# Kernel tuning notes

Measured on AMD Instinct MI355X. Metric: run time of the kernel, lower is better.

Reference implementation:

```python
import jax, jax.numpy as jnp
import numpy as np

N, E, G = 50000, 500000, 32
H, D = 4, 40  # heads, per-head dim; hidden = H*D = 160
HID, JK = H * D, 2 * H * D  # 160, 320


def setup_inputs() -> dict:
    key = jax.random.key(0)
    ks = jax.random.split(key, 32)
    s = 0.05
    inp = {
        'x': jax.random.normal(ks[0], (N, 5), jnp.float32),
        'edge_index': jax.random.randint(ks[1], (2, E), 0, N, jnp.int32).astype(jnp.int64),
        'edge_attr': jax.random.normal(ks[2], (E, 4), jnp.float32),
        'batch': jnp.sort(jax.random.randint(ks[3], (N,), 0, G, jnp.int32)).astype(jnp.int64),
        'W_in': jax.random.normal(ks[4], (5, HID), jnp.float32) * s,
        'b_in': jnp.zeros((HID,), jnp.float32),
        'Wq': jax.random.normal(ks[5], (2, HID, HID), jnp.float32) * s,
        'bq': jnp.zeros((2, HID), jnp.float32),
        'Wk': jax.random.normal(ks[6], (2, HID, HID), jnp.float32) * s,
        'bk': jnp.zeros((2, HID), jnp.float32),
        'Wv': jax.random.normal(ks[7], (2, HID, HID), jnp.float32) * s,
        'bv': jnp.zeros((2, HID), jnp.float32),
        'We': jax.random.normal(ks[8], (2, 4, HID), jnp.float32) * s,
        'be': jnp.zeros((2, HID), jnp.float32),
        'Wskip': jax.random.normal(ks[9], (2, HID, HID), jnp.float32) * s,
        'bskip': jnp.zeros((2, HID), jnp.float32),
        'Wbeta': jax.random.normal(ks[10], (2, 3 * HID, 1), jnp.float32) * s,
        'Wg1': jax.random.normal(ks[11], (JK, JK // 2), jnp.float32) * s,
        'bg1': jnp.zeros((JK // 2,), jnp.float32),
        'Wg2': jax.random.normal(ks[12], (JK // 2, 1), jnp.float32) * s,
        'bg2': jnp.zeros((1,), jnp.float32),
        'Wh1': jax.random.normal(ks[13], (JK, JK), jnp.float32) * s,
        'bh1': jnp.zeros((JK,), jnp.float32),
        'Wh2': jax.random.normal(ks[14], (JK, 6), jnp.float32) * s,
        'bh2': jnp.zeros((6,), jnp.float32),
    }
    return inp


def _transformer_conv(h, src, dst, edge_attr, Wq, bq, Wk, bk, Wv, bv, We, be, Wskip, bskip, Wbeta):
    n = h.shape[0]
    q = (h @ Wq + bq).reshape(n, H, D)
    k = (h @ Wk + bk).reshape(n, H, D)
    v = (h @ Wv + bv).reshape(n, H, D)
    e = (edge_attr @ We + be).reshape(-1, H, D)   # [E,H,D]
    k_e = k[src] + e                              # key with edge feature
    v_e = v[src] + e                              # value with edge feature
    alpha = jnp.einsum('ehd,ehd->eh', q[dst], k_e) / jnp.sqrt(jnp.float32(D))  # [E,H]
    # segment softmax over incoming edges of each destination node
    amax = jax.ops.segment_max(alpha, dst, num_segments=n)
    ex = jnp.exp(alpha - amax[dst])
    denom = jax.ops.segment_sum(ex, dst, num_segments=n)
    a = ex / denom[dst]                           # [E,H]
    out = jax.ops.segment_sum(v_e * a[..., None], dst, num_segments=n).reshape(n, H * D)
    # beta gate with skip connection
    r = h @ Wskip + bskip
    beta = jax.nn.sigmoid(jnp.concatenate([out, r, out - r], axis=-1) @ Wbeta)  # [n,1]
    return beta * r + (1.0 - beta) * out


def reference(x, edge_index, edge_attr, batch, W_in, b_in, Wq, bq, Wk, bk, Wv, bv,
              We, be, Wskip, bskip, Wbeta, Wg1, bg1, Wg2, bg2, Wh1, bh1, Wh2, bh2):
    src, dst = edge_index[0], edge_index[1]
    h = x @ W_in + b_in
    xs = []
    for l in range(2):
        h = _transformer_conv(h, src, dst, edge_attr, Wq[l], bq[l], Wk[l], bk[l],
                              Wv[l], bv[l], We[l], be[l], Wskip[l], bskip[l], Wbeta[l])
        xs.append(h)
    xc = jnp.concatenate(xs, axis=-1)             # JumpingKnowledge 'cat' -> [N,320]
    # AttentionalAggregation: gate MLP + segment softmax over graphs
    gate = jax.nn.relu(xc @ Wg1 + bg1) @ Wg2 + bg2  # [N,1]
    gmax = jax.ops.segment_max(gate, batch, num_segments=G)
    ge = jnp.exp(gate - gmax[batch])
    gden = jax.ops.segment_sum(ge, batch, num_segments=G)
    att = ge / gden[batch]
    pooled = jax.ops.segment_sum(att * xc, batch, num_segments=G)  # [G,320]
    out = jax.nn.relu(pooled @ Wh1 + bh1) @ Wh2 + bh2              # [G,6]
    return out.reshape(-1, 2, 3)
```

## Files before the change

### kernel.cpp

```cpp
#include <hip/hip_runtime.h>
#include <math.h>
#include <stddef.h>

#define NHEAD 4
#define DHEAD 40
#define HIDW 160
#define JKW 320
#define NGRAPH 32
#define BCAP 64

typedef __attribute__((ext_vector_type(8))) short short8;
typedef __attribute__((ext_vector_type(4))) float f32x4;
typedef __attribute__((ext_vector_type(2))) float f32x2;
typedef __fp16 h2 __attribute__((ext_vector_type(2)));
typedef int i32x4 __attribute__((ext_vector_type(4)));
typedef i32x4 i32x4_a4 __attribute__((aligned(4)));

__device__ inline unsigned short f2bf(float x){
  unsigned u = __float_as_uint(x);
  u += 0x7fff + ((u >> 16) & 1);
  return (unsigned short)(u >> 16);
}
__device__ inline float bf2f(unsigned short h){
  return __uint_as_float(((unsigned)h) << 16);
}
__device__ inline float fdot2(h2 a, h2 b, float c){
  return __builtin_amdgcn_fdot2(a, b, c, false);
}
__device__ inline h2 pk(float a, float b){
  return __builtin_amdgcn_cvt_pkrtz(a, b);
}
union HU { h2 h; int i; unsigned u; float f; };
__device__ inline h2 shfl_h2(h2 v, int xm){
  HU u; u.h = v; u.i = __shfl_xor(u.i, xm); return u.h;
}
__device__ inline h2 asH2(unsigned i){ HU u; u.u = i; return u.h; }

#if __has_builtin(__builtin_amdgcn_cvt_pk_f16_fp8)
__device__ inline h2 cvt8(int s){ return __builtin_amdgcn_cvt_pk_f16_fp8((short)s); }
#else
__device__ inline h2 cvt8(int s){
  f32x2 t = __builtin_amdgcn_cvt_pk_f32_fp8(s, false);
  return pk(t.x, t.y);
}
#endif

__device__ inline int lbound(const int* __restrict__ b, int N, int g){
  int lo = 0, hi = N;
  while (lo < hi){ int mid = (lo + hi) >> 1; if (b[mid] < g) lo = mid + 1; else hi = mid; }
  return lo;
}

__global__ __launch_bounds__(256) void k_pre(const float* __restrict__ x, const float* __restrict__ W_in,
                                             const float* __restrict__ b_in, unsigned short* __restrict__ hb,
                                             const float* __restrict__ Wq, const float* __restrict__ Wk,
                                             const float* __restrict__ Wv, const float* __restrict__ Ws,
                                             const float* __restrict__ bq, const float* __restrict__ bk,
                                             const float* __restrict__ bv, const float* __restrict__ bs,
                                             const float* __restrict__ Wg1,
                                             unsigned short* __restrict__ Bth, float* __restrict__ bp,
                                             unsigned short* __restrict__ Btgh,
                                             int* __restrict__ cnt, float* __restrict__ gate,
                                             float* __restrict__ pooled, int N){
  int NL = (N*20 + 255)/256;
  int bid = blockIdx.x, tid = threadIdx.x;
  if (bid < NL){
    int idx = bid*256 + tid;
    if (idx >= N*20) return;
    int n = idx / 20, j8 = (idx % 20)*8;
    const float* xr = x + n*5;
    float x0 = xr[0], x1 = xr[1], x2 = xr[2], x3 = xr[3], x4 = xr[4];
    float v[8];
    #pragma unroll
    for (int u = 0; u < 8; ++u) v[u] = b_in[j8+u];
    #pragma unroll
    for (int c = 0; c < 5; ++c){
      float xc = (c==0)?x0:(c==1)?x1:(c==2)?x2:(c==3)?x3:x4;
      const float4 wa = *(const float4*)(W_in + c*HIDW + j8);
      const float4 wb = *(const float4*)(W_in + c*HIDW + j8 + 4);
      v[0] += xc*wa.x; v[1] += xc*wa.y; v[2] += xc*wa.z; v[3] += xc*wa.w;
      v[4] += xc*wb.x; v[5] += xc*wb.y; v[6] += xc*wb.z; v[7] += xc*wb.w;
    }
    short8 o;
    #pragma unroll
    for (int u = 0; u < 8; ++u) o[u] = (short)f2bf(v[u]);
    *(short8*)(hb + (size_t)n*JKW + j8) = o;
  } else if (bid < NL + 1005){
    int idx = (bid - NL)*256 + tid;
    if (idx < 204800){
      int l = idx / 102400, r = idx % 102400;
      int i = r / 640, j = r % 640;
      int sel = j / HIDW, jj = j % HIDW;
      const float* W = (sel==0) ? Wq : (sel==1) ? Wk : (sel==2) ? Wv : Ws;
      Bth[(size_t)l*102400 + (size_t)j*160 + i] = f2bf(W[(size_t)l*25600 + i*HIDW + jj]);
    } else if (idx < 256000){
      int r = idx - 204800;
      int j = r / 320, i = r % 320;
      Btgh[(size_t)j*320 + i] = f2bf(Wg1[(size_t)i*160 + j]);
    } else if (idx < 257280){
      int r = idx - 256000;
      int l = r / 640, j = r % 640;
      int sel = j / HIDW, jj = j % HIDW;
      const float* bb = (sel==0) ? bq : (sel==1) ? bk : (sel==2) ? bv : bs;
      bp[l*640 + j] = bb[l*160 + jj];
    }
  } else {
    int idx = (bid - NL - 1005)*256 + tid;
    if (idx < N){ cnt[idx] = 0; gate[idx] = 0.f; }
    if (idx < NGRAPH*JKW) pooled[idx] = 0.f;
  }
}

__global__ __launch_bounds__(256) void k_fill(const int* __restrict__ dst, const int* __restrict__ src,
                                              const float* __restrict__ edge_attr, int E,
                                              int* __restrict__ cnt, uint4* __restrict__ edges){
  int e = blockIdx.x*256 + threadIdx.x;
  if (e < E){
    int d = dst[e];
    int p = atomicAdd(&cnt[d], 1);
    if (p < BCAP){
      float4 ea = *(const float4*)(edge_attr + (size_t)e*4);
      HU a, b; a.h = pk(ea.x, ea.y); b.h = pk(ea.z, ea.w);
      edges[(size_t)d*BCAP + p] = make_uint4((unsigned)src[e], a.u, b.u, 0u);
    }
  }
}

#define BSTR 40
#define BSTR1 164
template<int NSUB, int MODE>
__global__ __launch_bounds__(256) void k_mgemm(const unsigned short* __restrict__ A, int lda,
                                               const unsigned short* __restrict__ Bh,
                                               const float* __restrict__ bias,
                                               _Float16* __restrict__ qh,
                                               unsigned char* __restrict__ kv8,
                                               _Float16* __restrict__ rskip,
                                               const float* __restrict__ Wg2,
                                               float* __restrict__ gate,
                                               int M, int K){
  __shared__ short sBh[(MODE==1) ? (16*NSUB*BSTR1) : (2*16*NSUB*BSTR)];
  int tid = threadIdx.x;
  int wv = tid >> 6, lane = tid & 63;
  int quad = lane >> 4, l16 = lane & 15;

  int P = gridDim.x, MBy = gridDim.y;
  int bid = blockIdx.y * P + blockIdx.x;
  int fullRows = (MBy >> 3) << 3;
  int rowB, panel;
  if (bid < fullRows * P){
    int group = bid / (8*P), rem = bid % (8*P);
    rowB  = group*8 + (rem & 7);
    panel = rem >> 3;
  } else {
    int rem = bid - fullRows*P;
    int R = MBy - fullRows;
    panel = rem / R;
    rowB  = fullRows + rem % R;
  }
  int m0 = rowB*128 + wv*32;
  int col0 = panel * (16*NSUB);

  int ar0 = m0 + l16;      if (ar0 >= M) ar0 = M - 1;
  int ar1 = m0 + 16 + l16; if (ar1 >= M) ar1 = M - 1;
  const unsigned short* Ap0 = A + (size_t)ar0*lda + quad*8;
  const unsigned short* Ap1 = A + (size_t)ar1*lda + quad*8;

  f32x4 acc[2][NSUB];
  #pragma unroll
  for (int g = 0; g < 2; ++g)
    #pragma unroll
    for (int s = 0; s < NSUB; ++s) acc[g][s] = (f32x4){0.f,0.f,0.f,0.f};

  if constexpr (MODE == 1){
    for (int u = tid; u < 16*NSUB*20; u += 256){
      int col = u / 20, q = u % 20;
      *(short8*)(&sBh[col*BSTR1 + q*8]) =
        *(const short8*)(Bh + (size_t)(col0 + col)*K + q*8);
    }
    __syncthreads();
    #pragma unroll
    for (int kk = 0; kk < 5; ++kk){
      int k0 = kk << 5;
      short8 ah0 = *(const short8*)(Ap0 + k0);
      short8 ah1 = *(const short8*)(Ap1 + k0);
      #pragma unroll
      for (int s = 0; s < NSUB; ++s){
        short8 bh = *(const short8*)(&sBh[(s*16 + l16)*BSTR1 + k0 + quad*8]);
        acc[0][s] = __builtin_amdgcn_mfma_f32_16x16x32_bf16(bh, ah0, acc[0][s], 0, 0, 0);
        acc[1][s] = __builtin_amdgcn_mfma_f32_16x16x32_bf16(bh, ah1, acc[1][s], 0, 0, 0);
      }
    }
  } else {
    const int CH = K >> 5;
    for (int u = tid; u < 16*NSUB*4; u += 256){
      int col = u >> 2, q4 = u & 3;
      *(short8*)(&sBh[col*BSTR + q4*8]) =
        *(const short8*)(Bh + (size_t)(col0 + col)*K + q4*8);
    }
    __syncthreads();
    int buf = 0;
    for (int kk = 0; kk < CH; ++kk){
      int k0 = kk << 5;
      if (kk + 1 < CH){
        int kn = k0 + 32;
        for (int u = tid; u < 16*NSUB*4; u += 256){
          int col = u >> 2, q4 = u & 3;
          *(short8*)(&sBh[(buf^1)*16*NSUB*BSTR + col*BSTR + q4*8]) =
            *(const short8*)(Bh + (size_t)(col0 + col)*K + kn + q4*8);
        }
      }
      short8 ah0 = *(const short8*)(Ap0 + k0);
      short8 ah1 = *(const short8*)(Ap1 + k0);
      #pragma unroll
      for (int s = 0; s < NSUB; ++s){
        short8 bh = *(const short8*)(&sBh[buf*16*NSUB*BSTR + (s*16 + l16)*BSTR + quad*8]);
        acc[0][s] = __builtin_amdgcn_mfma_f32_16x16x32_bf16(bh, ah0, acc[0][s], 0, 0, 0);
        acc[1][s] = __builtin_amdgcn_mfma_f32_16x16x32_bf16(bh, ah1, acc[1][s], 0, 0, 0);
      }
      __syncthreads();
      buf ^= 1;
    }
  }

  const float qscale = 0.15811388300841898f;
  if (MODE == 1){
    #pragma unroll
    for (int g = 0; g < 2; ++g){
      int row = m0 + g*16 + l16;
      if (row >= M) continue;
      #pragma unroll
      for (int s = 0; s < NSUB; ++s){
        int col4 = col0 + s*16 + quad*4;
        int sel = col4 / 160, cc4 = col4 % 160;
        const float4 bv = *(const float4*)(bias + col4);
        float v0 = acc[g][s][0] + bv.x;
        float v1 = acc[g][s][1] + bv.y;
        float v2 = acc[g][s][2] + bv.z;
        float v3 = acc[g][s][3] + bv.w;
        if (sel == 0){
          HU a, b; a.h = pk(v0*qscale, v1*qscale); b.h = pk(v2*qscale, v3*qscale);
          *(uint2*)(qh + (size_t)row*160 + cc4) = make_uint2(a.u, b.u);
        } else if (sel == 3){
          HU a, b; a.h = pk(v0, v1); b.h = pk(v2, v3);
          *(uint2*)(rskip + (size_t)row*160 + cc4) = make_uint2(a.u, b.u);
        } else {
          int slot = (cc4/40)*4 + (cc4%40)/10, j = cc4%10;
          int off = (sel==2) ? 10 : 0;
          unsigned short e01 = (unsigned short)(__builtin_amdgcn_cvt_pk_fp8_f32(v0, v1, 0, false) & 0xffff);
          unsigned short e23 = (unsigned short)(__builtin_amdgcn_cvt_pk_fp8_f32(v2, v3, 0, false) & 0xffff);
          unsigned char* base = kv8 + (size_t)row*320;
          if (j <= 6){
            *(unsigned short*)(base + slot*20 + off + j)     = e01;
            *(unsigned short*)(base + slot*20 + off + j + 2) = e23;
          } else {
            *(unsigned short*)(base + slot*20 + off + 8)     = e01;
            *(unsigned short*)(base + (slot+1)*20 + off + 0) = e23;
          }
        }
      }
    }
  } else {
    float vg0 = 0.f, vg1 = 0.f;
    #pragma unroll
    for (int s = 0; s < NSUB; ++s){
      int col4 = col0 + s*16 + quad*4;
      const float4 bv = *(const float4*)(bias + col4);
      const float4 wg = *(const float4*)(Wg2 + col4);
      vg0 += fmaxf(acc[0][s][0]+bv.x,0.f)*wg.x + fmaxf(acc[0][s][1]+bv.y,0.f)*wg.y
           + fmaxf(acc[0][s][2]+bv.z,0.f)*wg.z + fmaxf(acc[0][s][3]+bv.w,0.f)*wg.w;
      vg1 += fmaxf(acc[1][s][0]+bv.x,0.f)*wg.x + fmaxf(acc[1][s][1]+bv.y,0.f)*wg.y
           + fmaxf(acc[1][s][2]+bv.z,0.f)*wg.z + fmaxf(acc[1][s][3]+bv.w,0.f)*wg.w;
    }
    vg0 += __shfl_xor(vg0, 16); vg0 += __shfl_xor(vg0, 32);
    vg1 += __shfl_xor(vg1, 16); vg1 += __shfl_xor(vg1, 32);
    if (quad == 0){
      int row0 = m0 + l16, row1 = m0 + 16 + l16;
      if (row0 < M) gate[row0] = vg0;
      if (row1 < M) gate[row1] = vg1;
    }
  }
}

__global__ __launch_bounds__(256) void k_qprep(const _Float16* __restrict__ qh,
                                               const float* __restrict__ We, const float* __restrict__ be,
                                               float* __restrict__ qwb, int N){
  int idx = blockIdx.x*256 + threadIdx.x;
  if (idx >= N*4) return;
  int n = idx >> 2, h = idx & 3;
  const unsigned* qp = (const unsigned*)(qh + (size_t)n*160 + h*40);
  float w0=0.f,w1=0.f,w2=0.f,w3=0.f,b=0.f;
  #pragma unroll
  for (int i = 0; i < 20; ++i){
    HU u; u.u = qp[i];
    float qa = (float)u.h.x, qb = (float)u.h.y;
    int c = h*40 + 2*i;
    w0 += qa*We[c]       + qb*We[c+1];
    w1 += qa*We[160+c]   + qb*We[161+c];
    w2 += qa*We[320+c]   + qb*We[321+c];
    w3 += qa*We[480+c]   + qb*We[481+c];
    b  += qa*be[c]       + qb*be[c+1];
  }
  float* o = qwb + (size_t)idx*5;
  o[0]=w0; o[1]=w1; o[2]=w2; o[3]=w3; o[4]=b;
}

__global__ __launch_bounds__(256) void k_attn(const _Float16* __restrict__ qh,
                                              const unsigned char* __restrict__ kv8,
                                              const _Float16* __restrict__ rskip,
                                              const float* __restrict__ qwb,
                                              const uint4* __restrict__ edges,
                                              const int* __restrict__ cnt,
                                              const float* __restrict__ We, const float* __restrict__ be,
                                              const float* __restrict__ Wb,
                                              unsigned short* __restrict__ hb,
                                              int loff, int N){
  int tid = threadIdx.x;
  int grp = tid >> 4;
  int n = blockIdx.x*16 + grp;
  bool valid = (n < N);
  int nn = valid ? n : (N-1);
  int w = tid & 15;
  int hh = w & 3, t = w >> 2;
  int cbase = DHEAD*hh + 10*t;
  int slot = hh*4 + t;

  h2 qh2[5];
  {
    const unsigned* qp = (const unsigned*)(qh + (size_t)nn*160 + cbase);
    #pragma unroll
    for (int i = 0; i < 5; ++i) qh2[i] = asH2(qp[i]);
  }
  const float* qwp = qwb + ((size_t)nn*4 + hh)*5;
  float qw0 = qwp[0], qw1 = qwp[1], qw2 = qwp[2], qw3 = qwp[3], qb = qwp[4];
  h2 qw01 = pk(qw0, qw1), qw23 = pk(qw2, qw3);

  float ssum = 0.f;
  h2 zh = pk(0.f, 0.f);
  h2 acch[5], sah[2];
  #pragma unroll
  for (int i = 0; i < 5; ++i) acch[i] = zh;
  sah[0] = zh; sah[1] = zh;

  int deg = 0;
  if (valid){ deg = cnt[nn]; if (deg > BCAP) deg = BCAP; }
  int st = nn*BCAP;

  uint4 r0 = make_uint4(0,0,0,0), r1 = make_uint4(0,0,0,0);
  uint4 r2 = make_uint4(0,0,0,0), r3 = make_uint4(0,0,0,0);
  i32x4 k0v = {0,0,0,0}, k1v = {0,0,0,0}; int k0e = 0, k1e = 0;
  if (deg > 0) r0 = edges[st];
  if (deg > 1) r1 = edges[st+1];
  if (deg > 2) r2 = edges[st+2];
  if (deg > 3) r3 = edges[st+3];
  if (deg > 0){
    const unsigned char* kp = kv8 + (size_t)r0.x*320 + slot*20;
    k0v = *(const i32x4_a4*)kp; k0e = *(const int*)(kp+16);
  }
  if (deg > 1){
    const unsigned char* kp = kv8 + (size_t)r1.x*320 + slot*20;
    k1v = *(const i32x4_a4*)kp; k1e = *(const int*)(kp+16);
  }

  for (int e = 0; e < deg; e += 2){
    uint4 n0 = make_uint4(0,0,0,0), n1 = make_uint4(0,0,0,0);
    if (e + 4 < deg) n0 = edges[st + e + 4];
    if (e + 5 < deg) n1 = edges[st + e + 5];
    i32x4 k2v = {0,0,0,0}, k3v = {0,0,0,0}; int k2e = 0, k3e = 0;
    if (e + 2 < deg){
      const unsigned char* kp = kv8 + (size_t)r2.x*320 + slot*20;
      k2v = *(const i32x4_a4*)kp; k2e = *(const int*)(kp+16);
    }
    if (e + 3 < deg){
      const unsigned char* kp = kv8 + (size_t)r3.x*320 + slot*20;
      k3v = *(const i32x4_a4*)kp; k3e = *(const int*)(kp+16);
    }
    bool v1 = (e + 1 < deg);
    h2 ea00 = asH2(r0.y), ea01 = asH2(r0.z);
    h2 ea10 = asH2(r1.y), ea11 = asH2(r1.z);
    float p0 = 0.f, p1 = 0.f;
    p0 = fdot2(qh2[0], cvt8(k0v.x), p0);       p1 = fdot2(qh2[0], cvt8(k1v.x), p1);
    p0 = fdot2(qh2[1], cvt8(k0v.x >> 16), p0); p1 = fdot2(qh2[1], cvt8(k1v.x >> 16), p1);
    p0 = fdot2(qh2[2], cvt8(k0v.y), p0);       p1 = fdot2(qh2[2], cvt8(k1v.y), p1);
    p0 = fdot2(qh2[3], cvt8(k0v.y >> 16), p0); p1 = fdot2(qh2[3], cvt8(k1v.y >> 16), p1);
    p0 = fdot2(qh2[4], cvt8(k0v.z), p0);       p1 = fdot2(qh2[4], cvt8(k1v.z), p1);
    p0 += __shfl_xor(p0, 4);                   p1 += __shfl_xor(p1, 4);
    p0 += __shfl_xor(p0, 8);                   p1 += __shfl_xor(p1, 8);
    p0 += qb;                                  p1 += qb;
    p0 = fdot2(ea00, qw01, p0);                p1 = fdot2(ea10, qw01, p1);
    p0 = fdot2(ea01, qw23, p0);                p1 = fdot2(ea11, qw23, p1);

    float ex0 = __expf(p0);
    float ex1 = v1 ? __expf(p1) : 0.f;
    ssum += ex0;
    ssum += ex1;
    h2 eh0 = pk(ex0, ex0), eh1 = pk(ex1, ex1);
    acch[0] += cvt8(k0v.z >> 16)*eh0;  acch[0] += cvt8(k1v.z >> 16)*eh1;
    acch[1] += cvt8(k0v.w)*eh0;        acch[1] += cvt8(k1v.w)*eh1;
    acch[2] += cvt8(k0v.w >> 16)*eh0;  acch[2] += cvt8(k1v.w >> 16)*eh1;
    acch[3] += cvt8(k0e)*eh0;          acch[3] += cvt8(k1e)*eh1;
    acch[4] += cvt8(k0e >> 16)*eh0;    acch[4] += cvt8(k1e >> 16)*eh1;
    sah[0] += ea00*eh0;                sah[0] += ea10*eh1;
    sah[1] += ea01*eh0;                sah[1] += ea11*eh1;

    r0 = r2; r1 = r3; r2 = n0; r3 = n1;
    k0v = k2v; k0e = k2e; k1v = k3v; k1e = k3e;
  }

  {
    float inv = (ssum > 0.f) ? 1.f/ssum : 0.f;
    float sw0 = (float)sah[0].x*inv, sw1 = (float)sah[0].y*inv;
    float sw2 = (float)sah[1].x*inv, sw3 = (float)sah[1].y*inv;
    float bterm = (ssum > 0.f) ? 1.f : 0.f;

    const unsigned* rpu = (const unsigned*)(rskip + (size_t)nn*160 + cbase);
    float o[10];
    float part = 0.f;
    #pragma unroll
    for (int i = 0; i < 5; ++i){
      int c = cbase + 2*i;
      float o0 = (float)acch[i].x*inv + sw0*We[c]   + sw1*We[160+c] + sw2*We[320+c] + sw3*We[480+c] + bterm*be[c];
      float o1 = (float)acch[i].y*inv + sw0*We[c+1] + sw1*We[161+c] + sw2*We[321+c] + sw3*We[481+c] + bterm*be[c+1];
      HU u; u.u = rpu[i];
      float r0f = (float)u.h.x, r1f = (float)u.h.y;
      part += o0*Wb[c]   + r0f*Wb[160+c] + (o0-r0f)*Wb[320+c];
      part += o1*Wb[c+1] + r1f*Wb[161+c] + (o1-r1f)*Wb[321+c];
      o[2*i] = o0; o[2*i+1] = o1;
    }
    part += __shfl_xor(part, 1); part += __shfl_xor(part, 2);
    part += __shfl_xor(part, 4); part += __shfl_xor(part, 8);
    float beta = 1.f/(1.f + __expf(-part));
    if (valid){
      unsigned* hp32 = (unsigned*)(hb + (size_t)nn*JKW + loff);
      #pragma unroll
      for (int i = 0; i < 5; ++i){
        HU u; u.u = rpu[i];
        float r0f = (float)u.h.x, r1f = (float)u.h.y;
        unsigned lo = f2bf(beta*r0f + (1.f-beta)*o[2*i]);
        unsigned hi = f2bf(beta*r1f + (1.f-beta)*o[2*i+1]);
        hp32[cbase/2 + i] = lo | (hi << 16);
      }
    }
  }
}

__global__ __launch_bounds__(256) void k_gatt(float* __restrict__ gate, const int* __restrict__ batch, int N){
  __shared__ float sm[256];
  int g = blockIdx.x, j = threadIdx.x;
  int lo = lbound(batch, N, g), hi = lbound(batch, N, g+1);
  if (hi <= lo) return;
  float m = -INFINITY;
  for (int i = lo + j; i < hi; i += 256) m = fmaxf(m, gate[i]);
  sm[j] = m; __syncthreads();
  #pragma unroll
  for (int off = 128; off; off >>= 1){
    if (j < off) sm[j] = fmaxf(sm[j], sm[j+off]);
    __syncthreads();
  }
  float gm = sm[0]; __syncthreads();
  float s = 0.f;
  for (int i = lo + j; i < hi; i += 256) s += __expf(gate[i] - gm);
  sm[j] = s; __syncthreads();
  #pragma unroll
  for (int off = 128; off; off >>= 1){
    if (j < off) sm[j] += sm[j+off];
    __syncthreads();
  }
  float dg = sm[0];
  float invd = (dg > 0.f) ? 1.f/dg : 0.f;
  for (int i = lo + j; i < hi; i += 256) gate[i] = __expf(gate[i] - gm) * invd;
}

__global__ __launch_bounds__(320) void k_pool(const unsigned short* __restrict__ hb, const float* __restrict__ gate,
                                              const int* __restrict__ batch, int N,
                                              float* __restrict__ pooled){
  int g = blockIdx.x, part = blockIdx.y, j = threadIdx.x;
  int lo = lbound(batch, N, g), hi = lbound(batch, N, g+1);
  int len = hi - lo;
  if (len <= 0) return;
  int chunk = (len + (int)gridDim.y - 1) / (int)gridDim.y;
  int a = lo + part*chunk;
  int bnd = a + chunk; if (bnd > hi) bnd = hi;
  if (a >= bnd) return;
  float acc = 0.f;
  #pragma unroll 2
  for (int n = a; n < bnd; ++n){
    acc += gate[n] * bf2f(hb[(size_t)n*JKW + j]);
  }
  atomicAdd(&pooled[g*JKW + j], acc);
}

__global__ __launch_bounds__(320) void k_head(const float* __restrict__ pooled, const float* __restrict__ Wh1,
                                              const float* __restrict__ bh1, const float* __restrict__ Wh2,
                                              const float* __restrict__ bh2, float* __restrict__ out){
  __shared__ float p[320];
  __shared__ float t[320];
  int g = blockIdx.x, tid = threadIdx.x;
  p[tid] = pooled[g*JKW + tid]; __syncthreads();
  float a = bh1[tid];
  for (int i = 0; i < 320; ++i) a += p[i]*Wh1[i*JKW + tid];
  t[tid] = fmaxf(a, 0.f); __syncthreads();
  if (tid < 6){
    float o = bh2[tid];
    for (int j = 0; j < 320; ++j) o += t[j]*Wh2[j*6 + tid];
    out[g*6 + tid] = o;
  }
}

extern "C" void kernel_launch(void* const* d_in, const int* in_sizes, int n_in,
                              void* d_out, int out_size, void* d_ws, size_t ws_size,
                              hipStream_t stream){
  (void)n_in; (void)out_size; (void)ws_size;
  const float* x        = (const float*)d_in[0];
  const int*   eidx     = (const int*)d_in[1];
  const float* edge_attr= (const float*)d_in[2];
  const int*   batch    = (const int*)d_in[3];
  const float* W_in     = (const float*)d_in[4];
  const float* b_in     = (const float*)d_in[5];
  const float* Wq       = (const float*)d_in[6];
  const float* bq       = (const float*)d_in[7];
  const float* Wk       = (const float*)d_in[8];
  const float* bk       = (const float*)d_in[9];
  const float* Wv       = (const float*)d_in[10];
  const float* bv       = (const float*)d_in[11];
  const float* We       = (const float*)d_in[12];
  const float* be       = (const float*)d_in[13];
  const float* Wsk      = (const float*)d_in[14];
  const float* bsk      = (const float*)d_in[15];
  const float* Wb       = (const float*)d_in[16];
  const float* Wg1      = (const float*)d_in[17];
  const float* bg1      = (const float*)d_in[18];
  const float* Wg2      = (const float*)d_in[19];
  const float* Wh1      = (const float*)d_in[21];
  const float* bh1      = (const float*)d_in[22];
  const float* Wh2      = (const float*)d_in[23];
  const float* bh2      = (const float*)d_in[24];

  const int N = in_sizes[0] / 5;
  const int E = in_sizes[1] / 2;
  float* out = (float*)d_out;

  char* w = (char*)d_ws;
  auto alloc = [&](size_t bytes)->char*{ char* p = w; w += (bytes + 255) & ~(size_t)255; return p; };
  unsigned short* hb = (unsigned short*)alloc((size_t)N*JKW*2);
  _Float16* qh  = (_Float16*)alloc((size_t)N*160*2);
  unsigned char* kv8 = (unsigned char*)alloc((size_t)N*320);
  _Float16* rskip = (_Float16*)alloc((size_t)N*160*2);
  float* qwb    = (float*)alloc((size_t)N*20*4);
  unsigned short* Bth  = (unsigned short*)alloc((size_t)2*640*160*2);
  unsigned short* Btgh = (unsigned short*)alloc((size_t)160*320*2);
  float* bpack  = (float*)alloc((size_t)2*640*4);
  int*   cnt    = (int*)alloc((size_t)N*4);
  uint4* edges  = (uint4*)alloc((size_t)N*BCAP*16);
  float* gate   = (float*)alloc((size_t)N*4);
  float* pooled = (float*)alloc(NGRAPH*JKW*4);

  const int* srcI = eidx;
  const int* dstI = eidx + E;

  const int NL = (N*20 + 255)/256;
  const int NZ = (N + 255)/256;
  k_pre<<<NL + 1005 + NZ, 256, 0, stream>>>(x, W_in, b_in, hb,
                                            Wq, Wk, Wv, Wsk, bq, bk, bv, bsk, Wg1,
                                            Bth, bpack, Btgh, cnt, gate, pooled, N);

  const int eb = (E + 255)/256;
  k_fill<<<eb, 256, 0, stream>>>(dstI, srcI, edge_attr, E, cnt, edges);

  const int MB128 = (N + 127)/128;
  for (int l = 0; l < 2; ++l){
    dim3 g1(10, MB128);
    k_mgemm<4,1><<<g1, 256, 0, stream>>>(hb, JKW, Bth + (size_t)l*102400, bpack + l*640,
                                         qh, kv8, rskip, nullptr, nullptr, N, HIDW);
    k_qprep<<<(N*4 + 255)/256, 256, 0, stream>>>(qh, We + l*640, be + l*160, qwb, N);
    k_attn<<<(N + 15)/16, 256, 0, stream>>>(qh, kv8, rskip, qwb, edges, cnt,
                                            We + l*640, be + l*160, Wb + l*480, hb, l*HIDW, N);
  }

  k_mgemm<10,2><<<dim3(1, MB128), 256, 0, stream>>>(hb, JKW, Btgh, bg1, nullptr, nullptr, nullptr,
                                                    Wg2, gate, N, JKW);

  k_gatt<<<NGRAPH, 256, 0, stream>>>(gate, batch, N);
  dim3 g3(NGRAPH, 32);
  k_pool<<<g3, 320, 0, stream>>>(hb, gate, batch, N, pooled);
  k_head<<<NGRAPH, 320, 0, stream>>>(pooled, Wh1, bh1, Wh2, bh2, out);
}
```

Before: 417.3 us.

## Fold q·We projections into the QKV GEMM weights and drop the qprep kernel

Precomputes Wq·We and bq·We products per head as 20 extra GEMM columns, padded to 768, so the per-node q-edge weights come straight out of the main projection GEMM. This removes the separate k_qprep kernel and its re-read of qh in each layer. The GEMM tile width changes from 4 to 8 sub-tiles over 6 panels to cover the wider output. In exchange the weight-prep work grows, 108 of the 768 columns are zero padding, and the folded products are rounded to bf16 before use.

```diff
diff --git a/kernel.cpp b/kernel.cpp
--- a/kernel.cpp
+++ b/kernel.cpp
@@ -8,6 +8,8 @@
 #define JKW 320
 #define NGRAPH 32
 #define BCAP 64
+#define BCOLS 768
+#define BREAL 660
 
 typedef __attribute__((ext_vector_type(8))) short short8;
 typedef __attribute__((ext_vector_type(4))) float f32x4;
@@ -58,10 +60,12 @@
                                              const float* __restrict__ bq, const float* __restrict__ bk,
                                              const float* __restrict__ bv, const float* __restrict__ bs,
                                              const float* __restrict__ Wg1,
+                                             const float* __restrict__ We, const float* __restrict__ be,
                                              unsigned short* __restrict__ Bth, float* __restrict__ bp,
                                              unsigned short* __restrict__ Btgh,
                                              int* __restrict__ cnt, float* __restrict__ gate,
                                              float* __restrict__ pooled, int N){
+  const float qscale = 0.15811388300841898f;
   int NL = (N*20 + 255)/256;
   int bid = blockIdx.x, tid = threadIdx.x;
   if (bid < NL){
@@ -85,27 +89,51 @@
     #pragma unroll
     for (int u = 0; u < 8; ++u) o[u] = (short)f2bf(v[u]);
     *(short8*)(hb + (size_t)n*JKW + j8) = o;
-  } else if (bid < NL + 1005){
+  } else if (bid < NL + 1166){
     int idx = (bid - NL)*256 + tid;
-    if (idx < 204800){
-      int l = idx / 102400, r = idx % 102400;
-      int i = r / 640, j = r % 640;
-      int sel = j / HIDW, jj = j % HIDW;
-      const float* W = (sel==0) ? Wq : (sel==1) ? Wk : (sel==2) ? Wv : Ws;
-      Bth[(size_t)l*102400 + (size_t)j*160 + i] = f2bf(W[(size_t)l*25600 + i*HIDW + jj]);
-    } else if (idx < 256000){
-      int r = idx - 204800;
+    if (idx < 2*BCOLS*160){
+      int l = idx / (BCOLS*160), r = idx % (BCOLS*160);
+      int i = r / BCOLS, j = r % BCOLS;
+      unsigned short outv;
+      if (j < 640){
+        int sel = j / HIDW, jj = j % HIDW;
+        const float* W = (sel==0) ? Wq : (sel==1) ? Wk : (sel==2) ? Wv : Ws;
+        outv = f2bf(W[(size_t)l*25600 + i*HIDW + jj]);
+      } else if (j < BREAL){
+        int c = j - 640, h = c / 5, rr = c % 5;
+        const float* wqr = Wq + (size_t)l*25600 + i*HIDW + 40*h;
+        const float* xr  = (rr < 4) ? (We + l*640 + rr*160 + 40*h) : (be + l*160 + 40*h);
+        float s = 0.f;
+        #pragma unroll
+        for (int d = 0; d < 40; ++d) s += wqr[d]*xr[d];
+        outv = f2bf(s * qscale);
+      } else outv = 0;
+      Bth[(size_t)l*(BCOLS*160) + (size_t)j*160 + i] = outv;
+    } else if (idx < 2*BCOLS*160 + 51200){
+      int r = idx - 2*BCOLS*160;
       int j = r / 320, i = r % 320;
       Btgh[(size_t)j*320 + i] = f2bf(Wg1[(size_t)i*160 + j]);
-    } else if (idx < 257280){
-      int r = idx - 256000;
-      int l = r / 640, j = r % 640;
-      int sel = j / HIDW, jj = j % HIDW;
-      const float* bb = (sel==0) ? bq : (sel==1) ? bk : (sel==2) ? bv : bs;
-      bp[l*640 + j] = bb[l*160 + jj];
+    } else if (idx < 2*BCOLS*160 + 51200 + 2*BCOLS){
+      int r = idx - (2*BCOLS*160 + 51200);
+      int l = r / BCOLS, j = r % BCOLS;
+      float bvv;
+      if (j < 640){
+        int sel = j / HIDW, jj = j % HIDW;
+        const float* b2 = (sel==0) ? bq : (sel==1) ? bk : (sel==2) ? bv : bs;
+        bvv = b2[l*160 + jj];
+      } else if (j < BREAL){
+        int c = j - 640, h = c / 5, rr = c % 5;
+        const float* bqr = bq + l*160 + 40*h;
+        const float* xr  = (rr < 4) ? (We + l*640 + rr*160 + 40*h) : (be + l*160 + 40*h);
+        float s = 0.f;
+        #pragma unroll
+        for (int d = 0; d < 40; ++d) s += bqr[d]*xr[d];
+        bvv = s * qscale;
+      } else bvv = 0.f;
+      bp[l*BCOLS + j] = bvv;
     }
   } else {
-    int idx = (bid - NL - 1005)*256 + tid;
+    int idx = (bid - NL - 1166)*256 + tid;
     if (idx < N){ cnt[idx] = 0; gate[idx] = 0.f; }
     if (idx < NGRAPH*JKW) pooled[idx] = 0.f;
   }
@@ -135,6 +163,7 @@
                                                _Float16* __restrict__ qh,
                                                unsigned char* __restrict__ kv8,
                                                _Float16* __restrict__ rskip,
+                                               float* __restrict__ qwb,
                                                const float* __restrict__ Wg2,
                                                float* __restrict__ gate,
                                                int M, int K){
@@ -243,6 +272,11 @@
         } else if (sel == 3){
           HU a, b; a.h = pk(v0, v1); b.h = pk(v2, v3);
           *(uint2*)(rskip + (size_t)row*160 + cc4) = make_uint2(a.u, b.u);
+        } else if (sel >= 4){
+          if (col4 < BREAL){
+            float4 o4; o4.x = v0; o4.y = v1; o4.z = v2; o4.w = v3;
+            *(float4*)(qwb + (size_t)row*20 + (col4 - 640)) = o4;
+          }
         } else {
           int slot = (cc4/40)*4 + (cc4%40)/10, j = cc4%10;
           int off = (sel==2) ? 10 : 0;
@@ -279,29 +313,6 @@
       if (row1 < M) gate[row1] = vg1;
     }
   }
-}
-
-__global__ __launch_bounds__(256) void k_qprep(const _Float16* __restrict__ qh,
-                                               const float* __restrict__ We, const float* __restrict__ be,
-                                               float* __restrict__ qwb, int N){
-  int idx = blockIdx.x*256 + threadIdx.x;
-  if (idx >= N*4) return;
-  int n = idx >> 2, h = idx & 3;
-  const unsigned* qp = (const unsigned*)(qh + (size_t)n*160 + h*40);
-  float w0=0.f,w1=0.f,w2=0.f,w3=0.f,b=0.f;
-  #pragma unroll
-  for (int i = 0; i < 20; ++i){
-    HU u; u.u = qp[i];
-    float qa = (float)u.h.x, qb = (float)u.h.y;
-    int c = h*40 + 2*i;
-    w0 += qa*We[c]       + qb*We[c+1];
-    w1 += qa*We[160+c]   + qb*We[161+c];
-    w2 += qa*We[320+c]   + qb*We[321+c];
-    w3 += qa*We[480+c]   + qb*We[481+c];
-    b  += qa*be[c]       + qb*be[c+1];
-  }
-  float* o = qwb + (size_t)idx*5;
-  o[0]=w0; o[1]=w1; o[2]=w2; o[3]=w3; o[4]=b;
 }
 
 __global__ __launch_bounds__(256) void k_attn(const _Float16* __restrict__ qh,
@@ -330,7 +341,7 @@
     #pragma unroll
     for (int i = 0; i < 5; ++i) qh2[i] = asH2(qp[i]);
   }
-  const float* qwp = qwb + ((size_t)nn*4 + hh)*5;
+  const float* qwp = qwb + (size_t)nn*20 + hh*5;
   float qw0 = qwp[0], qw1 = qwp[1], qw2 = qwp[2], qw3 = qwp[3], qb = qwp[4];
   h2 qw01 = pk(qw0, qw1), qw23 = pk(qw2, qw3);
 
@@ -546,9 +557,9 @@
   unsigned char* kv8 = (unsigned char*)alloc((size_t)N*320);
   _Float16* rskip = (_Float16*)alloc((size_t)N*160*2);
   float* qwb    = (float*)alloc((size_t)N*20*4);
-  unsigned short* Bth  = (unsigned short*)alloc((size_t)2*640*160*2);
+  unsigned short* Bth  = (unsigned short*)alloc((size_t)2*BCOLS*160*2);
   unsigned short* Btgh = (unsigned short*)alloc((size_t)160*320*2);
-  float* bpack  = (float*)alloc((size_t)2*640*4);
+  float* bpack  = (float*)alloc((size_t)2*BCOLS*4);
   int*   cnt    = (int*)alloc((size_t)N*4);
   uint4* edges  = (uint4*)alloc((size_t)N*BCAP*16);
   float* gate   = (float*)alloc((size_t)N*4);
@@ -559,8 +570,8 @@
 
   const int NL = (N*20 + 255)/256;
   const int NZ = (N + 255)/256;
-  k_pre<<<NL + 1005 + NZ, 256, 0, stream>>>(x, W_in, b_in, hb,
-                                            Wq, Wk, Wv, Wsk, bq, bk, bv, bsk, Wg1,
+  k_pre<<<NL + 1166 + NZ, 256, 0, stream>>>(x, W_in, b_in, hb,
+                                            Wq, Wk, Wv, Wsk, bq, bk, bv, bsk, Wg1, We, be,
                                             Bth, bpack, Btgh, cnt, gate, pooled, N);
 
   const int eb = (E + 255)/256;
@@ -568,15 +579,14 @@
 
   const int MB128 = (N + 127)/128;
   for (int l = 0; l < 2; ++l){
-    dim3 g1(10, MB128);
-    k_mgemm<4,1><<<g1, 256, 0, stream>>>(hb, JKW, Bth + (size_t)l*102400, bpack + l*640,
-                                         qh, kv8, rskip, nullptr, nullptr, N, HIDW);
-    k_qprep<<<(N*4 + 255)/256, 256, 0, stream>>>(qh, We + l*640, be + l*160, qwb, N);
+    dim3 g1(6, MB128);
+    k_mgemm<8,1><<<g1, 256, 0, stream>>>(hb, JKW, Bth + (size_t)l*(BCOLS*160), bpack + l*BCOLS,
+                                         qh, kv8, rskip, qwb, nullptr, nullptr, N, HIDW);
     k_attn<<<(N + 15)/16, 256, 0, stream>>>(qh, kv8, rskip, qwb, edges, cnt,
                                             We + l*640, be + l*160, Wb + l*480, hb, l*HIDW, N);
   }
 
-  k_mgemm<10,2><<<dim3(1, MB128), 256, 0, stream>>>(hb, JKW, Btgh, bg1, nullptr, nullptr, nullptr,
+  k_mgemm<10,2><<<dim3(1, MB128), 256, 0, stream>>>(hb, JKW, Btgh, bg1, nullptr, nullptr, nullptr, nullptr,
                                                     Wg2, gate, N, JKW);
 
   k_gatt<<<NGRAPH, 256, 0, stream>>>(gate, batch, N);
```

Result: faster. 402.0 us, median of 3 (-3.7%).
